# Kernel tuning notes

Measured on AMD Instinct MI355X. Metric: run time of the kernel, lower is better.

The kernel has to match this reference:

```python
import jax, jax.numpy as jnp
import numpy as np

EMBED_DIM = 1024
NUM_HEADS = 16
HEAD_DIM = EMBED_DIM // NUM_HEADS


def setup_inputs() -> dict:
    key = jax.random.key(0)
    k_x, k_wqkv, k_bqkv, k_wo, k_bo = jax.random.split(key, 5)
    B, S, D = 4, 2048, EMBED_DIM
    x = jax.random.normal(k_x, (B, S, D), dtype=jnp.float32)
    # Dense(embed_dim*3): weight [D, 3D], bias [3D]
    w_qkv = jax.random.normal(k_wqkv, (D, 3 * D), dtype=jnp.float32) * (1.0 / np.sqrt(D))
    b_qkv = jnp.zeros((3 * D,), dtype=jnp.float32)
    # Dense(embed_dim): weight [D, D], bias [D]
    w_out = jax.random.normal(k_wo, (D, D), dtype=jnp.float32) * (1.0 / np.sqrt(D))
    b_out = jnp.zeros((D,), dtype=jnp.float32)
    return {"x": x, "w_qkv": w_qkv, "b_qkv": b_qkv, "w_out": w_out, "b_out": b_out}


def reference(x, w_qkv, b_qkv, w_out, b_out):
    B, S, D = x.shape
    H, Hd = NUM_HEADS, HEAD_DIM
    qkv = x @ w_qkv + b_qkv                      # [B, S, 3D]
    qkv = qkv.reshape(B, S, 3, H, Hd)
    qkv = jnp.transpose(qkv, (2, 0, 3, 1, 4))    # [3, B, H, S, Hd]
    q, k, v = qkv[0], qkv[1], qkv[2]
    scores = jnp.einsum('bhqd,bhkd->bhqk', q, k) / jnp.sqrt(jnp.float32(Hd))
    # causal mask: lower-triangular ones, applied as scores*mask + (1-mask)*(-1e9)
    mask = jnp.tril(jnp.ones((S, S), dtype=jnp.float32))[None, None]
    scores = scores * mask + (1.0 - mask) * -1e9
    attn = jax.nn.softmax(scores, axis=-1)       # [B, H, S, S]
    out = jnp.einsum('bhqk,bhkd->bhqd', attn, v) # [B, H, S, Hd]
    out = jnp.transpose(out, (0, 2, 1, 3)).reshape(B, S, D)
    return out @ w_out + b_out
```

## Files before the change

### kernel.cpp

```cpp
#include <hip/hip_runtime.h>
#include <hip/hip_bf16.h>

#define NUMH 16
#define HD   64
#define EMB  1024
#define SEQL 2048
#define BATCH 4

typedef __attribute__((ext_vector_type(8))) short bf16x8;
typedef __attribute__((ext_vector_type(4))) float f32x4;
typedef __attribute__((ext_vector_type(16))) float f32x16;

__device__ __forceinline__ unsigned short f2bf(float f) {
  union { float f; unsigned int u; } v; v.f = f;
  unsigned int u = v.u + 0x7fffu + ((v.u >> 16) & 1u);
  return (unsigned short)(u >> 16);
}

__device__ __forceinline__ unsigned int cvtpk(float lo, float hi) {
  unsigned int r;
  asm("v_cvt_pk_bf16_f32 %0, %1, %2" : "=v"(r) : "v"(lo), "v"(hi));
  return r;
}

__device__ __forceinline__ float xhalf_max(float x) {
#if __has_builtin(__builtin_amdgcn_permlane32_swap)
  auto r = __builtin_amdgcn_permlane32_swap(__float_as_uint(x), __float_as_uint(x), false, false);
  return fmaxf(__uint_as_float(r[0]), __uint_as_float(r[1]));
#else
  return fmaxf(x, __shfl_xor(x, 32));
#endif
}
__device__ __forceinline__ float xhalf_sum(float x) {
#if __has_builtin(__builtin_amdgcn_permlane32_swap)
  auto r = __builtin_amdgcn_permlane32_swap(__float_as_uint(x), __float_as_uint(x), false, false);
  return __uint_as_float(r[0]) + __uint_as_float(r[1]);
#else
  return x + __shfl_xor(x, 32);
#endif
}

#define GLOAD16(gp, lp)                                                        \
  __builtin_amdgcn_global_load_lds(                                            \
      (const __attribute__((address_space(1))) unsigned int*)(gp),             \
      (__attribute__((address_space(3))) unsigned int*)(lp), 16, 0, 0)

__global__ __launch_bounds__(256) void cvt_x(const float* __restrict__ src,
                                             unsigned short* __restrict__ dst) {
  const size_t i = ((size_t)blockIdx.x * 256 + threadIdx.x) * 8;
  float4 a = *(const float4*)(src + i);
  float4 b = *(const float4*)(src + i + 4);
  bf16x8 w;
  w[0]=(short)f2bf(a.x); w[1]=(short)f2bf(a.y); w[2]=(short)f2bf(a.z); w[3]=(short)f2bf(a.w);
  w[4]=(short)f2bf(b.x); w[5]=(short)f2bf(b.y); w[6]=(short)f2bf(b.z); w[7]=(short)f2bf(b.w);
  *(bf16x8*)(dst + i) = w;
}

__global__ __launch_bounds__(256) void tr_cvt(const float* __restrict__ src,
                                              unsigned short* __restrict__ dst,
                                              int R, int C) {
  __shared__ unsigned short t[32][34];
  const int tx = threadIdx.x & 31, ty = threadIdx.x >> 5;
  const int c0 = blockIdx.x * 32, r0 = blockIdx.y * 32;
#pragma unroll
  for (int i = 0; i < 4; ++i)
    t[ty + i * 8][tx] = f2bf(src[(size_t)(r0 + ty + i * 8) * C + c0 + tx]);
  __syncthreads();
#pragma unroll
  for (int i = 0; i < 4; ++i)
    dst[(size_t)(c0 + ty + i * 8) * R + r0 + tx] = t[tx][ty + i * 8];
}

__global__ __launch_bounds__(256, 3) void gemm_qkv(
    const unsigned short* __restrict__ A, const unsigned short* __restrict__ BT,
    const float* __restrict__ Bias,
    unsigned short* __restrict__ Qo, unsigned short* __restrict__ Ko,
    unsigned short* __restrict__ Vo) {
  __shared__ __align__(16) unsigned short As[128][32];
  __shared__ __align__(16) unsigned short Bs[128][32];
  const int tid = threadIdx.x, lane = tid & 63, wv = tid >> 6;
  const int l15 = lane & 15, lg = lane >> 4;
  const int wrow = (wv >> 1) * 64, wcol = (wv & 1) * 64;
  const int cpx = gridDim.x >> 3;
  const int wg = (blockIdx.x & 7) * cpx + (blockIdx.x >> 3);
  const int mbase = (wg / 24) * 128, nbase = (wg % 24) * 128;

  f32x4 acc[4][4];
#pragma unroll
  for (int i = 0; i < 4; ++i)
#pragma unroll
    for (int j = 0; j < 4; ++j) acc[i][j] = (f32x4){0.f, 0.f, 0.f, 0.f};

  const int c0 = wv * 64 + lane;
  const unsigned short* ga0 = A + (size_t)(mbase + (c0 >> 2)) * EMB + (c0 & 3) * 8;
  const unsigned short* ga1 = ga0 + (size_t)64 * EMB;
  const unsigned short* gb0 = BT + (size_t)(nbase + (c0 >> 2)) * EMB + (c0 & 3) * 8;
  const unsigned short* gb1 = gb0 + (size_t)64 * EMB;
  unsigned short* la0 = &As[0][0] + c0 * 8;
  unsigned short* lb0 = &Bs[0][0] + c0 * 8;

  for (int k0 = 0; k0 < EMB; k0 += 32) {
    __syncthreads();
    GLOAD16(ga0 + k0, la0);
    GLOAD16(ga1 + k0, la0 + 2048);
    GLOAD16(gb0 + k0, lb0);
    GLOAD16(gb1 + k0, lb0 + 2048);
    __syncthreads();
    bf16x8 af[4], bfr[4];
#pragma unroll
    for (int mf = 0; mf < 4; ++mf)
      af[mf] = *(const bf16x8*)&As[wrow + mf * 16 + l15][lg * 8];
#pragma unroll
    for (int nf = 0; nf < 4; ++nf)
      bfr[nf] = *(const bf16x8*)&Bs[wcol + nf * 16 + l15][lg * 8];
#pragma unroll
    for (int mf = 0; mf < 4; ++mf)
#pragma unroll
      for (int nf = 0; nf < 4; ++nf)
        acc[mf][nf] = __builtin_amdgcn_mfma_f32_16x16x32_bf16(af[mf], bfr[nf], acc[mf][nf], 0, 0, 0);
  }

#pragma unroll
  for (int nf = 0; nf < 4; ++nf) {
    const int n = nbase + wcol + nf * 16 + l15;
    const float bias = Bias[n];
    const int which = n >> 10, rem = n & 1023;
    const int h = rem >> 6, d = rem & 63;
    unsigned short* dst = (which == 0) ? Qo : (which == 1) ? Ko : Vo;
#pragma unroll
    for (int mf = 0; mf < 4; ++mf)
#pragma unroll
      for (int j = 0; j < 4; ++j) {
        const int m = mbase + wrow + mf * 16 + lg * 4 + j;
        const int bb = m >> 11, s = m & 2047;
        dst[((size_t)(bb * NUMH + h) * SEQL + s) * HD + d] = f2bf(acc[mf][nf][j] + bias);
      }
  }
}

__global__ __launch_bounds__(256, 3) void gemm_out(
    const unsigned short* __restrict__ A, const unsigned short* __restrict__ BT,
    const float* __restrict__ Bias, float* __restrict__ Out) {
  __shared__ __align__(16) unsigned short As[128][32];
  __shared__ __align__(16) unsigned short Bs[128][32];
  const int tid = threadIdx.x, lane = tid & 63, wv = tid >> 6;
  const int l15 = lane & 15, lg = lane >> 4;
  const int wrow = (wv >> 1) * 64, wcol = (wv & 1) * 64;
  const int cpx = gridDim.x >> 3;
  const int wg = (blockIdx.x & 7) * cpx + (blockIdx.x >> 3);
  const int mbase = (wg >> 3) * 128, nbase = (wg & 7) * 128;

  f32x4 acc[4][4];
#pragma unroll
  for (int i = 0; i < 4; ++i)
#pragma unroll
    for (int j = 0; j < 4; ++j) acc[i][j] = (f32x4){0.f, 0.f, 0.f, 0.f};

  const int c0 = wv * 64 + lane;
  const unsigned short* ga0 = A + (size_t)(mbase + (c0 >> 2)) * EMB + (c0 & 3) * 8;
  const unsigned short* ga1 = ga0 + (size_t)64 * EMB;
  const unsigned short* gb0 = BT + (size_t)(nbase + (c0 >> 2)) * EMB + (c0 & 3) * 8;
  const unsigned short* gb1 = gb0 + (size_t)64 * EMB;
  unsigned short* la0 = &As[0][0] + c0 * 8;
  unsigned short* lb0 = &Bs[0][0] + c0 * 8;

  for (int k0 = 0; k0 < EMB; k0 += 32) {
    __syncthreads();
    GLOAD16(ga0 + k0, la0);
    GLOAD16(ga1 + k0, la0 + 2048);
    GLOAD16(gb0 + k0, lb0);
    GLOAD16(gb1 + k0, lb0 + 2048);
    __syncthreads();
    bf16x8 af[4], bfr[4];
#pragma unroll
    for (int mf = 0; mf < 4; ++mf)
      af[mf] = *(const bf16x8*)&As[wrow + mf * 16 + l15][lg * 8];
#pragma unroll
    for (int nf = 0; nf < 4; ++nf)
      bfr[nf] = *(const bf16x8*)&Bs[wcol + nf * 16 + l15][lg * 8];
#pragma unroll
    for (int mf = 0; mf < 4; ++mf)
#pragma unroll
      for (int nf = 0; nf < 4; ++nf)
        acc[mf][nf] = __builtin_amdgcn_mfma_f32_16x16x32_bf16(af[mf], bfr[nf], acc[mf][nf], 0, 0, 0);
  }

#pragma unroll
  for (int nf = 0; nf < 4; ++nf) {
    const int n = nbase + wcol + nf * 16 + l15;
    const float bias = Bias[n];
#pragma unroll
    for (int mf = 0; mf < 4; ++mf)
#pragma unroll
      for (int j = 0; j < 4; ++j) {
        const int m = mbase + wrow + mf * 16 + lg * 4 + j;
        Out[(size_t)m * EMB + n] = acc[mf][nf][j] + bias;
      }
  }
}

__device__ __forceinline__ void sm_pack(f32x16& S0, f32x16& S1, float& MR, float& LR,
                                        f32x16& O0, f32x16& O1, bf16x8 Pf[4],
                                        int ktb, int qrow, int q0w, int hi) {
  const float AS = 0.18033688011112042f;
  const float THRR = 44.36f;
  if (ktb + 63 > q0w) {
#pragma unroll
    for (int r = 0; r < 16; ++r) {
      const int kv0 = ktb + (r & 3) + 8 * (r >> 2) + 4 * hi;
      S0[r] = (kv0 > qrow) ? -1e30f : S0[r];
      S1[r] = (kv0 + 32 > qrow) ? -1e30f : S1[r];
    }
  }
  float t[16];
#pragma unroll
  for (int i = 0; i < 16; ++i) t[i] = fmaxf(S0[i], S1[i]);
#pragma unroll
  for (int i = 0; i < 8; ++i) t[i] = fmaxf(t[i], t[i + 8]);
#pragma unroll
  for (int i = 0; i < 4; ++i) t[i] = fmaxf(t[i], t[i + 4]);
  float mx = fmaxf(fmaxf(t[0], t[1]), fmaxf(t[2], t[3]));
  mx = xhalf_max(mx);
  if (!__all(mx - MR <= THRR)) {
    const float mn = fmaxf(MR, mx);
    const float sc = exp2f((MR - mn) * AS);
    MR = mn;
    LR *= sc;
#pragma unroll
    for (int i = 0; i < 16; ++i) { O0[i] *= sc; O1[i] *= sc; }
  }
  const float mk = MR * AS;
#pragma unroll
  for (int i = 0; i < 16; ++i) {
    S0[i] = exp2f(__builtin_fmaf(S0[i], AS, -mk));
    S1[i] = exp2f(__builtin_fmaf(S1[i], AS, -mk));
  }
  float a[16];
#pragma unroll
  for (int i = 0; i < 16; ++i) a[i] = S0[i] + S1[i];
#pragma unroll
  for (int i = 0; i < 8; ++i) a[i] += a[i + 8];
#pragma unroll
  for (int i = 0; i < 4; ++i) a[i] += a[i + 4];
  LR += xhalf_sum((a[0] + a[1]) + (a[2] + a[3]));
  unsigned int W[2][4][2], X[2][4][2];
#pragma unroll
  for (int g = 0; g < 4; ++g)
#pragma unroll
    for (int c = 0; c < 2; ++c) {
      W[0][g][c] = cvtpk(S0[4 * g + 2 * c], S0[4 * g + 2 * c + 1]);
      W[1][g][c] = cvtpk(S1[4 * g + 2 * c], S1[4 * g + 2 * c + 1]);
    }
#pragma unroll
  for (int tt = 0; tt < 2; ++tt)
#pragma unroll
    for (int g = 0; g < 4; ++g)
#pragma unroll
      for (int c = 0; c < 2; ++c) X[tt][g][c] = __shfl_xor(W[tt][g][c], 32);

#pragma unroll
  for (int ks = 0; ks < 4; ++ks) {
    const int tt = ks >> 1, k1 = ks & 1;
    union { unsigned int d[4]; bf16x8 v; } u;
    u.d[0] = hi ? X[tt][2 * k1 + 1][0] : W[tt][2 * k1][0];
    u.d[1] = hi ? X[tt][2 * k1 + 1][1] : W[tt][2 * k1][1];
    u.d[2] = hi ? W[tt][2 * k1 + 1][0] : X[tt][2 * k1][0];
    u.d[3] = hi ? W[tt][2 * k1 + 1][1] : X[tt][2 * k1][1];
    Pf[ks] = u.v;
  }
}

__device__ __forceinline__ void write_o(unsigned short* Op, const f32x16& O0,
                                        const f32x16& O1, float LR, int hi) {
  const float inv = 1.0f / LR;
#pragma unroll
  for (int g = 0; g < 4; ++g) {
    unsigned int w00 = cvtpk(O0[4 * g] * inv, O0[4 * g + 1] * inv);
    unsigned int w01 = cvtpk(O0[4 * g + 2] * inv, O0[4 * g + 3] * inv);
    unsigned int w10 = cvtpk(O1[4 * g] * inv, O1[4 * g + 1] * inv);
    unsigned int w11 = cvtpk(O1[4 * g + 2] * inv, O1[4 * g + 3] * inv);
    const int dd = 8 * g + 4 * hi;
    *(uint2*)&Op[dd]      = uint2{w00, w01};
    *(uint2*)&Op[32 + dd] = uint2{w10, w11};
  }
}

__global__ __launch_bounds__(256, 2) void attn_fwd(
    const unsigned short* __restrict__ Q, const unsigned short* __restrict__ K,
    const unsigned short* __restrict__ V, unsigned short* __restrict__ O) {
  __shared__ __align__(16) unsigned short Ks[64][72];
  __shared__ __align__(16) unsigned short VT[64][72];
  const int tid = threadIdx.x, lane = tid & 63, wv = tid >> 6;
  const int l31 = lane & 31, hi = lane >> 5;
  const int d0 = blockIdx.x;
  const int qp = (d0 >> 3) & 7;
  const int bh = ((d0 & 7) << 3) | (d0 >> 6);
  const int b = bh >> 4, h = bh & 15;
  const size_t bho = (size_t)(b * NUMH + h) * SEQL * HD;
  const unsigned short* Qb = Q + bho;
  const unsigned short* Kb = K + bho;
  const unsigned short* Vb = V + bho;

  const int qtA = qp, qtB = 15 - qp;
  const int q0wA = qtA * 128 + wv * 32, q0wB = qtB * 128 + wv * 32;
  const int qrowA = q0wA + l31, qrowB = q0wB + l31;

  const int skrow = tid >> 2, skcol = (tid & 3) * 16;
  const int svrow = tid & 63, svd = (tid >> 6) * 16;

  bf16x8 qfA[4], qfB[4];
#pragma unroll
  for (int s = 0; s < 4; ++s) {
    qfA[s] = *(const bf16x8*)&Qb[(size_t)qrowA * HD + s * 16 + hi * 8];
    qfB[s] = *(const bf16x8*)&Qb[(size_t)qrowB * HD + s * 16 + hi * 8];
  }

  f32x16 OA0, OA1, OB0, OB1;
#pragma unroll
  for (int i = 0; i < 16; ++i) { OA0[i] = 0.f; OA1[i] = 0.f; OB0[i] = 0.f; OB1[i] = 0.f; }
  float mA = -1e30f, lA = 0.f, mB = -1e30f, lB = 0.f;

  const int nkt = 2 * qtB + 2;
  for (int kt = 0; kt < nkt; ++kt) {
    const int ktb = kt * 64;
    __syncthreads();
    {
      const unsigned short* kp = &Kb[(size_t)(ktb + skrow) * HD + skcol];
      *(uint4*)&Ks[skrow][skcol] = *(const uint4*)kp;
      *(uint4*)&Ks[skrow][skcol + 8] = *(const uint4*)(kp + 8);
    }
    {
      const unsigned short* vp = &Vb[(size_t)(ktb + svrow) * HD + svd];
      union { uint4 u[2]; unsigned short s[16]; } vb;
      vb.u[0] = *(const uint4*)vp;
      vb.u[1] = *(const uint4*)(vp + 8);
#pragma unroll
      for (int i = 0; i < 16; ++i) VT[svd + i][svrow] = vb.s[i];
    }
    __syncthreads();

    const bool aAct = (ktb <= q0wA + 31);
    const bool bAct = (ktb <= q0wB + 31);

    f32x16 SA0, SA1, SB0, SB1;
    if (bAct) {
#pragma unroll
      for (int i = 0; i < 16; ++i) { SB0[i] = 0.f; SB1[i] = 0.f; }
    }
    if (aAct) {
#pragma unroll
      for (int i = 0; i < 16; ++i) { SA0[i] = 0.f; SA1[i] = 0.f; }
    }
#pragma unroll
    for (int s = 0; s < 4; ++s) {
      bf16x8 kf0 = *(const bf16x8*)&Ks[l31][s * 16 + hi * 8];
      bf16x8 kf1 = *(const bf16x8*)&Ks[32 + l31][s * 16 + hi * 8];
      if (bAct) {
        SB0 = __builtin_amdgcn_mfma_f32_32x32x16_bf16(kf0, qfB[s], SB0, 0, 0, 0);
        SB1 = __builtin_amdgcn_mfma_f32_32x32x16_bf16(kf1, qfB[s], SB1, 0, 0, 0);
      }
      if (aAct) {
        SA0 = __builtin_amdgcn_mfma_f32_32x32x16_bf16(kf0, qfA[s], SA0, 0, 0, 0);
        SA1 = __builtin_amdgcn_mfma_f32_32x32x16_bf16(kf1, qfA[s], SA1, 0, 0, 0);
      }
    }

    bf16x8 PfA[4], PfB[4];
    if (aAct) sm_pack(SA0, SA1, mA, lA, OA0, OA1, PfA, ktb, qrowA, q0wA, hi);
    if (bAct) sm_pack(SB0, SB1, mB, lB, OB0, OB1, PfB, ktb, qrowB, q0wB, hi);

#pragma unroll
    for (int ks = 0; ks < 4; ++ks) {
      bf16x8 vf0 = *(const bf16x8*)&VT[l31][ks * 16 + hi * 8];
      bf16x8 vf1 = *(const bf16x8*)&VT[32 + l31][ks * 16 + hi * 8];
      if (bAct) {
        OB0 = __builtin_amdgcn_mfma_f32_32x32x16_bf16(vf0, PfB[ks], OB0, 0, 0, 0);
        OB1 = __builtin_amdgcn_mfma_f32_32x32x16_bf16(vf1, PfB[ks], OB1, 0, 0, 0);
      }
      if (aAct) {
        OA0 = __builtin_amdgcn_mfma_f32_32x32x16_bf16(vf0, PfA[ks], OA0, 0, 0, 0);
        OA1 = __builtin_amdgcn_mfma_f32_32x32x16_bf16(vf1, PfA[ks], OA1, 0, 0, 0);
      }
    }
  }

  write_o(O + ((size_t)b * SEQL + qrowA) * EMB + h * HD, OA0, OA1, lA, hi);
  write_o(O + ((size_t)b * SEQL + qrowB) * EMB + h * HD, OB0, OB1, lB, hi);
}

extern "C" void kernel_launch(void* const* d_in, const int* in_sizes, int n_in,
                              void* d_out, int out_size, void* d_ws, size_t ws_size,
                              hipStream_t stream) {
  const float* x     = (const float*)d_in[0];
  const float* w_qkv = (const float*)d_in[1];
  const float* b_qkv = (const float*)d_in[2];
  const float* w_out = (const float*)d_in[3];
  const float* b_out = (const float*)d_in[4];
  float* out = (float*)d_out;

  const size_t NE = (size_t)BATCH * NUMH * SEQL * HD;
  unsigned short* Qb = (unsigned short*)d_ws;
  unsigned short* Kb = Qb + NE;
  unsigned short* Vb = Kb + NE;
  unsigned short* AO = Vb + NE;
  unsigned short* xb = AO + NE;
  unsigned short* wqkvT = xb + NE;
  unsigned short* woutT = wqkvT + 3072 * 1024;

  cvt_x<<<dim3((unsigned)(NE / (256 * 8))), 256, 0, stream>>>(x, xb);
  tr_cvt<<<dim3(3072 / 32, 1024 / 32), 256, 0, stream>>>(w_qkv, wqkvT, 1024, 3072);
  tr_cvt<<<dim3(1024 / 32, 1024 / 32), 256, 0, stream>>>(w_out, woutT, 1024, 1024);

  gemm_qkv<<<dim3(1536), 256, 0, stream>>>(xb, wqkvT, b_qkv, Qb, Kb, Vb);
  attn_fwd<<<dim3(512), 256, 0, stream>>>(Qb, Kb, Vb, AO);
  gemm_out<<<dim3(512), 256, 0, stream>>>(AO, woutT, b_out, out);
}
```

Measured before the change: 297.7 us.

## Double GEMM K-tile with XOR-swizzled LDS and split attention into one q-tile per block

Both GEMMs now load a 64-wide K slice per iteration into XOR-swizzled LDS. This halves the number of barrier pairs and is meant to avoid bank conflicts on the fragment reads. The attention kernel drops the paired light/heavy q-tile scheme and gives each block a single 128-row q tile, heaviest tiles first. It launches 1024 blocks with a launch bound allowing 4 blocks per CU, which raises occupancy and cuts register pressure. The trade-off is less K/V reuse per LDS load, and load balance now depends on scheduling order rather than explicit pairing.

Measured after the change: 263.0 us. 1.13x faster.

```diff
diff --git a/kernel.cpp b/kernel.cpp
--- a/kernel.cpp
+++ b/kernel.cpp
@@ -76,8 +76,8 @@
     const float* __restrict__ Bias,
     unsigned short* __restrict__ Qo, unsigned short* __restrict__ Ko,
     unsigned short* __restrict__ Vo) {
-  __shared__ __align__(16) unsigned short As[128][32];
-  __shared__ __align__(16) unsigned short Bs[128][32];
+  __shared__ __align__(16) unsigned short As[128][64];
+  __shared__ __align__(16) unsigned short Bs[128][64];
   const int tid = threadIdx.x, lane = tid & 63, wv = tid >> 6;
   const int l15 = lane & 15, lg = lane >> 4;
   const int wrow = (wv >> 1) * 64, wcol = (wv & 1) * 64;
@@ -91,33 +91,37 @@
 #pragma unroll
     for (int j = 0; j < 4; ++j) acc[i][j] = (f32x4){0.f, 0.f, 0.f, 0.f};
 
-  const int c0 = wv * 64 + lane;
-  const unsigned short* ga0 = A + (size_t)(mbase + (c0 >> 2)) * EMB + (c0 & 3) * 8;
-  const unsigned short* ga1 = ga0 + (size_t)64 * EMB;
-  const unsigned short* gb0 = BT + (size_t)(nbase + (c0 >> 2)) * EMB + (c0 & 3) * 8;
-  const unsigned short* gb1 = gb0 + (size_t)64 * EMB;
-  unsigned short* la0 = &As[0][0] + c0 * 8;
-  unsigned short* lb0 = &Bs[0][0] + c0 * 8;
-
-  for (int k0 = 0; k0 < EMB; k0 += 32) {
-    __syncthreads();
-    GLOAD16(ga0 + k0, la0);
-    GLOAD16(ga1 + k0, la0 + 2048);
-    GLOAD16(gb0 + k0, lb0);
-    GLOAD16(gb1 + k0, lb0 + 2048);
-    __syncthreads();
-    bf16x8 af[4], bfr[4];
-#pragma unroll
-    for (int mf = 0; mf < 4; ++mf)
-      af[mf] = *(const bf16x8*)&As[wrow + mf * 16 + l15][lg * 8];
-#pragma unroll
-    for (int nf = 0; nf < 4; ++nf)
-      bfr[nf] = *(const bf16x8*)&Bs[wcol + nf * 16 + l15][lg * 8];
-#pragma unroll
-    for (int mf = 0; mf < 4; ++mf)
+  const int row0 = tid >> 3;
+  const int scc = (tid & 7) ^ (row0 & 7);
+  const unsigned short* gA0 = A + (size_t)(mbase + row0) * EMB + scc * 8;
+  const unsigned short* gB0 = BT + (size_t)(nbase + row0) * EMB + scc * 8;
+  unsigned short* lA0 = &As[0][0] + tid * 8;
+  unsigned short* lB0 = &Bs[0][0] + tid * 8;
+
+  for (int k0 = 0; k0 < EMB; k0 += 64) {
+    __syncthreads();
+#pragma unroll
+    for (int i = 0; i < 4; ++i) {
+      GLOAD16(gA0 + (size_t)(32 * i) * EMB + k0, lA0 + 2048 * i);
+      GLOAD16(gB0 + (size_t)(32 * i) * EMB + k0, lB0 + 2048 * i);
+    }
+    __syncthreads();
+#pragma unroll
+    for (int ks2 = 0; ks2 < 2; ++ks2) {
+      bf16x8 af[4], bfr[4];
+      const int cc = ((ks2 * 4 + lg) ^ (l15 & 7)) * 8;
+#pragma unroll
+      for (int mf = 0; mf < 4; ++mf)
+        af[mf] = *(const bf16x8*)&As[wrow + mf * 16 + l15][cc];
 #pragma unroll
       for (int nf = 0; nf < 4; ++nf)
-        acc[mf][nf] = __builtin_amdgcn_mfma_f32_16x16x32_bf16(af[mf], bfr[nf], acc[mf][nf], 0, 0, 0);
+        bfr[nf] = *(const bf16x8*)&Bs[wcol + nf * 16 + l15][cc];
+#pragma unroll
+      for (int mf = 0; mf < 4; ++mf)
+#pragma unroll
+        for (int nf = 0; nf < 4; ++nf)
+          acc[mf][nf] = __builtin_amdgcn_mfma_f32_16x16x32_bf16(af[mf], bfr[nf], acc[mf][nf], 0, 0, 0);
+    }
   }
 
 #pragma unroll
@@ -141,8 +145,8 @@
 __global__ __launch_bounds__(256, 3) void gemm_out(
     const unsigned short* __restrict__ A, const unsigned short* __restrict__ BT,
     const float* __restrict__ Bias, float* __restrict__ Out) {
-  __shared__ __align__(16) unsigned short As[128][32];
-  __shared__ __align__(16) unsigned short Bs[128][32];
+  __shared__ __align__(16) unsigned short As[128][64];
+  __shared__ __align__(16) unsigned short Bs[128][64];
   const int tid = threadIdx.x, lane = tid & 63, wv = tid >> 6;
   const int l15 = lane & 15, lg = lane >> 4;
   const int wrow = (wv >> 1) * 64, wcol = (wv & 1) * 64;
@@ -156,33 +160,37 @@
 #pragma unroll
     for (int j = 0; j < 4; ++j) acc[i][j] = (f32x4){0.f, 0.f, 0.f, 0.f};
 
-  const int c0 = wv * 64 + lane;
-  const unsigned short* ga0 = A + (size_t)(mbase + (c0 >> 2)) * EMB + (c0 & 3) * 8;
-  const unsigned short* ga1 = ga0 + (size_t)64 * EMB;
-  const unsigned short* gb0 = BT + (size_t)(nbase + (c0 >> 2)) * EMB + (c0 & 3) * 8;
-  const unsigned short* gb1 = gb0 + (size_t)64 * EMB;
-  unsigned short* la0 = &As[0][0] + c0 * 8;
-  unsigned short* lb0 = &Bs[0][0] + c0 * 8;
-
-  for (int k0 = 0; k0 < EMB; k0 += 32) {
-    __syncthreads();
-    GLOAD16(ga0 + k0, la0);
-    GLOAD16(ga1 + k0, la0 + 2048);
-    GLOAD16(gb0 + k0, lb0);
-    GLOAD16(gb1 + k0, lb0 + 2048);
-    __syncthreads();
-    bf16x8 af[4], bfr[4];
-#pragma unroll
-    for (int mf = 0; mf < 4; ++mf)
-      af[mf] = *(const bf16x8*)&As[wrow + mf * 16 + l15][lg * 8];
-#pragma unroll
-    for (int nf = 0; nf < 4; ++nf)
-      bfr[nf] = *(const bf16x8*)&Bs[wcol + nf * 16 + l15][lg * 8];
-#pragma unroll
-    for (int mf = 0; mf < 4; ++mf)
+  const int row0 = tid >> 3;
+  const int scc = (tid & 7) ^ (row0 & 7);
+  const unsigned short* gA0 = A + (size_t)(mbase + row0) * EMB + scc * 8;
+  const unsigned short* gB0 = BT + (size_t)(nbase + row0) * EMB + scc * 8;
+  unsigned short* lA0 = &As[0][0] + tid * 8;
+  unsigned short* lB0 = &Bs[0][0] + tid * 8;
+
+  for (int k0 = 0; k0 < EMB; k0 += 64) {
+    __syncthreads();
+#pragma unroll
+    for (int i = 0; i < 4; ++i) {
+      GLOAD16(gA0 + (size_t)(32 * i) * EMB + k0, lA0 + 2048 * i);
+      GLOAD16(gB0 + (size_t)(32 * i) * EMB + k0, lB0 + 2048 * i);
+    }
+    __syncthreads();
+#pragma unroll
+    for (int ks2 = 0; ks2 < 2; ++ks2) {
+      bf16x8 af[4], bfr[4];
+      const int cc = ((ks2 * 4 + lg) ^ (l15 & 7)) * 8;
+#pragma unroll
+      for (int mf = 0; mf < 4; ++mf)
+        af[mf] = *(const bf16x8*)&As[wrow + mf * 16 + l15][cc];
 #pragma unroll
       for (int nf = 0; nf < 4; ++nf)
-        acc[mf][nf] = __builtin_amdgcn_mfma_f32_16x16x32_bf16(af[mf], bfr[nf], acc[mf][nf], 0, 0, 0);
+        bfr[nf] = *(const bf16x8*)&Bs[wcol + nf * 16 + l15][cc];
+#pragma unroll
+      for (int mf = 0; mf < 4; ++mf)
+#pragma unroll
+        for (int nf = 0; nf < 4; ++nf)
+          acc[mf][nf] = __builtin_amdgcn_mfma_f32_16x16x32_bf16(af[mf], bfr[nf], acc[mf][nf], 0, 0, 0);
+    }
   }
 
 #pragma unroll
@@ -285,42 +293,38 @@
   }
 }
 
-__global__ __launch_bounds__(256, 2) void attn_fwd(
+__global__ __launch_bounds__(256, 4) void attn_fwd(
     const unsigned short* __restrict__ Q, const unsigned short* __restrict__ K,
     const unsigned short* __restrict__ V, unsigned short* __restrict__ O) {
   __shared__ __align__(16) unsigned short Ks[64][72];
   __shared__ __align__(16) unsigned short VT[64][72];
   const int tid = threadIdx.x, lane = tid & 63, wv = tid >> 6;
   const int l31 = lane & 31, hi = lane >> 5;
-  const int d0 = blockIdx.x;
-  const int qp = (d0 >> 3) & 7;
-  const int bh = ((d0 & 7) << 3) | (d0 >> 6);
+  const int qt = 15 - (blockIdx.x >> 6);
+  const int bh = blockIdx.x & 63;
   const int b = bh >> 4, h = bh & 15;
   const size_t bho = (size_t)(b * NUMH + h) * SEQL * HD;
   const unsigned short* Qb = Q + bho;
   const unsigned short* Kb = K + bho;
   const unsigned short* Vb = V + bho;
 
-  const int qtA = qp, qtB = 15 - qp;
-  const int q0wA = qtA * 128 + wv * 32, q0wB = qtB * 128 + wv * 32;
-  const int qrowA = q0wA + l31, qrowB = q0wB + l31;
+  const int q0w = qt * 128 + wv * 32;
+  const int qrow = q0w + l31;
 
   const int skrow = tid >> 2, skcol = (tid & 3) * 16;
   const int svrow = tid & 63, svd = (tid >> 6) * 16;
 
-  bf16x8 qfA[4], qfB[4];
-#pragma unroll
-  for (int s = 0; s < 4; ++s) {
-    qfA[s] = *(const bf16x8*)&Qb[(size_t)qrowA * HD + s * 16 + hi * 8];
-    qfB[s] = *(const bf16x8*)&Qb[(size_t)qrowB * HD + s * 16 + hi * 8];
-  }
-
-  f32x16 OA0, OA1, OB0, OB1;
-#pragma unroll
-  for (int i = 0; i < 16; ++i) { OA0[i] = 0.f; OA1[i] = 0.f; OB0[i] = 0.f; OB1[i] = 0.f; }
-  float mA = -1e30f, lA = 0.f, mB = -1e30f, lB = 0.f;
-
-  const int nkt = 2 * qtB + 2;
+  bf16x8 qf[4];
+#pragma unroll
+  for (int s = 0; s < 4; ++s)
+    qf[s] = *(const bf16x8*)&Qb[(size_t)qrow * HD + s * 16 + hi * 8];
+
+  f32x16 O0, O1;
+#pragma unroll
+  for (int i = 0; i < 16; ++i) { O0[i] = 0.f; O1[i] = 0.f; }
+  float m_run = -1e30f, l_run = 0.f;
+
+  const int nkt = 2 * qt + 2;
   for (int kt = 0; kt < nkt; ++kt) {
     const int ktb = kt * 64;
     __syncthreads();
@@ -339,53 +343,30 @@
     }
     __syncthreads();
 
-    const bool aAct = (ktb <= q0wA + 31);
-    const bool bAct = (ktb <= q0wB + 31);
-
-    f32x16 SA0, SA1, SB0, SB1;
-    if (bAct) {
-#pragma unroll
-      for (int i = 0; i < 16; ++i) { SB0[i] = 0.f; SB1[i] = 0.f; }
-    }
-    if (aAct) {
-#pragma unroll
-      for (int i = 0; i < 16; ++i) { SA0[i] = 0.f; SA1[i] = 0.f; }
-    }
-#pragma unroll
-    for (int s = 0; s < 4; ++s) {
-      bf16x8 kf0 = *(const bf16x8*)&Ks[l31][s * 16 + hi * 8];
-      bf16x8 kf1 = *(const bf16x8*)&Ks[32 + l31][s * 16 + hi * 8];
-      if (bAct) {
-        SB0 = __builtin_amdgcn_mfma_f32_32x32x16_bf16(kf0, qfB[s], SB0, 0, 0, 0);
-        SB1 = __builtin_amdgcn_mfma_f32_32x32x16_bf16(kf1, qfB[s], SB1, 0, 0, 0);
+    if (ktb <= q0w + 31) {
+      f32x16 S0, S1;
+#pragma unroll
+      for (int i = 0; i < 16; ++i) { S0[i] = 0.f; S1[i] = 0.f; }
+#pragma unroll
+      for (int s = 0; s < 4; ++s) {
+        bf16x8 kf0 = *(const bf16x8*)&Ks[l31][s * 16 + hi * 8];
+        bf16x8 kf1 = *(const bf16x8*)&Ks[32 + l31][s * 16 + hi * 8];
+        S0 = __builtin_amdgcn_mfma_f32_32x32x16_bf16(kf0, qf[s], S0, 0, 0, 0);
+        S1 = __builtin_amdgcn_mfma_f32_32x32x16_bf16(kf1, qf[s], S1, 0, 0, 0);
       }
-      if (aAct) {
-        SA0 = __builtin_amdgcn_mfma_f32_32x32x16_bf16(kf0, qfA[s], SA0, 0, 0, 0);
-        SA1 = __builtin_amdgcn_mfma_f32_32x32x16_bf16(kf1, qfA[s], SA1, 0, 0, 0);
+      bf16x8 Pf[4];
+      sm_pack(S0, S1, m_run, l_run, O0, O1, Pf, ktb, qrow, q0w, hi);
+#pragma unroll
+      for (int ks = 0; ks < 4; ++ks) {
+        bf16x8 vf0 = *(const bf16x8*)&VT[l31][ks * 16 + hi * 8];
+        bf16x8 vf1 = *(const bf16x8*)&VT[32 + l31][ks * 16 + hi * 8];
+        O0 = __builtin_amdgcn_mfma_f32_32x32x16_bf16(vf0, Pf[ks], O0, 0, 0, 0);
+        O1 = __builtin_amdgcn_mfma_f32_32x32x16_bf16(vf1, Pf[ks], O1, 0, 0, 0);
       }
     }
-
-    bf16x8 PfA[4], PfB[4];
-    if (aAct) sm_pack(SA0, SA1, mA, lA, OA0, OA1, PfA, ktb, qrowA, q0wA, hi);
-    if (bAct) sm_pack(SB0, SB1, mB, lB, OB0, OB1, PfB, ktb, qrowB, q0wB, hi);
-
-#pragma unroll
-    for (int ks = 0; ks < 4; ++ks) {
-      bf16x8 vf0 = *(const bf16x8*)&VT[l31][ks * 16 + hi * 8];
-      bf16x8 vf1 = *(const bf16x8*)&VT[32 + l31][ks * 16 + hi * 8];
-      if (bAct) {
-        OB0 = __builtin_amdgcn_mfma_f32_32x32x16_bf16(vf0, PfB[ks], OB0, 0, 0, 0);
-        OB1 = __builtin_amdgcn_mfma_f32_32x32x16_bf16(vf1, PfB[ks], OB1, 0, 0, 0);
-      }
-      if (aAct) {
-        OA0 = __builtin_amdgcn_mfma_f32_32x32x16_bf16(vf0, PfA[ks], OA0, 0, 0, 0);
-        OA1 = __builtin_amdgcn_mfma_f32_32x32x16_bf16(vf1, PfA[ks], OA1, 0, 0, 0);
-      }
-    }
-  }
-
-  write_o(O + ((size_t)b * SEQL + qrowA) * EMB + h * HD, OA0, OA1, lA, hi);
-  write_o(O + ((size_t)b * SEQL + qrowB) * EMB + h * HD, OB0, OB1, lB, hi);
+  }
+
+  write_o(O + ((size_t)b * SEQL + qrow) * EMB + h * HD, O0, O1, l_run, hi);
 }
 
 extern "C" void kernel_launch(void* const* d_in, const int* in_sizes, int n_in,
@@ -412,6 +393,6 @@
   tr_cvt<<<dim3(1024 / 32, 1024 / 32), 256, 0, stream>>>(w_out, woutT, 1024, 1024);
 
   gemm_qkv<<<dim3(1536), 256, 0, stream>>>(xb, wqkvT, b_qkv, Qb, Kb, Vb);
-  attn_fwd<<<dim3(512), 256, 0, stream>>>(Qb, Kb, Vb, AO);
+  attn_fwd<<<dim3(1024), 256, 0, stream>>>(Qb, Kb, Vb, AO);
   gemm_out<<<dim3(512), 256, 0, stream>>>(AO, woutT, b_out, out);
 }
```
